# Performance work log

Measured on AMD Instinct MI355X. Metric: run time of the kernel, lower is better.

The kernel has to match this reference:

```python
import jax, jax.numpy as jnp
import numpy as np

NUM_LAYERS = 6
KS = 5  # kernel_size; also attention window size K
EPS_IN = 1e-5  # torch InstanceNorm1d default eps


def _conv1d(x, w, b, d, p):
    # x: [N,C,L], w: [O,I,KS], dilated 'same' conv
    y = jax.lax.conv_general_dilated(x, w, window_strides=(1,), padding=[(p, p)],
                                     rhs_dilation=(d,), dimension_numbers=('NCH', 'OIH', 'NCH'))
    return y + b[None, :, None]


def _pw(x, w, b):
    # pointwise (1x1) conv: x [N,C,L], w [O,C]
    return jnp.einsum('oc,ncl->nol', w, x) + b[None, :, None]


def _layer(x, x_cross, pr, d):
    C, L = x.shape[1], x.shape[2]
    p = (KS // 2) * d  # padding
    conv_w, conv_b, qw, qb, kw, kb, vw, vb, f1w, f1b, f2w, f2b = pr
    out1 = _conv1d(x, conv_w, conv_b, d, p)
    xc = jnp.concatenate([x, x_cross], axis=1)
    q = _pw(xc, qw, qb)            # [N,C,L]
    k = _pw(xc, kw, kb)
    v = _pw(x, vw, vb)
    kp = jnp.pad(k, ((0, 0), (0, 0), (p, p)))
    vp = jnp.pad(v, ((0, 0), (0, 0), (p, p)))
    # attn index for query q, slot j is (q + j*d) into padded axis -> shifted slices
    win_k = jnp.stack([kp[:, :, j * d:j * d + L] for j in range(KS)], axis=-1)  # [N,C,L,K]
    win_v = jnp.stack([vp[:, :, j * d:j * d + L] for j in range(KS)], axis=-1)
    att = jnp.einsum('ncl,nclk->nlk', q, win_k) / np.float32(np.sqrt(C))
    pos = jnp.arange(L)[:, None] + (jnp.arange(KS)[None, :] - KS // 2) * d  # absolute key pos
    mask = (pos >= 0) & (pos < L)  # [L,K]
    att = jax.nn.softmax(att + jnp.log(mask + 1e-6), axis=-1) * mask
    r = jnp.einsum('nlk,nclk->ncl', att, win_v)
    h = out1 + r
    # InstanceNorm1d (no affine): normalize over L per (n,c)
    mu = jnp.mean(h, axis=2, keepdims=True)
    var = jnp.var(h, axis=2, keepdims=True)
    h = (h - mu) * jax.lax.rsqrt(var + EPS_IN)
    out = _pw(jax.nn.relu(_pw(h, f1w, f1b)), f2w, f2b)
    return x + out


def reference(x, x_cross, time_emb, time_w, time_b, conv_w, conv_b, qw, qb, kw, kb, vw, vb, f1w, f1b, f2w, f2b):
    te = time_emb * jax.nn.sigmoid(time_emb)  # swish
    x = x + (te @ time_w.T + time_b)[:, :, None]
    for i in range(NUM_LAYERS):
        pr = (conv_w[i], conv_b[i], qw[i], qb[i], kw[i], kb[i], vw[i], vb[i],
              f1w[i], f1b[i], f2w[i], f2b[i])
        x = _layer(x, x_cross, pr, 2 ** i)
    return x


def setup_inputs() -> dict:
    N, C, CC, L, T, nL = 4, 256, 256, 4096, 512, NUM_LAYERS
    key = jax.random.key(0)
    ks = jax.random.split(key, 18)
    s = 0.05
    return {
        'x': jax.random.normal(ks[0], (N, C, L), jnp.float32),
        'x_cross': jax.random.normal(ks[1], (N, CC, L), jnp.float32),
        'time_emb': jax.random.normal(ks[2], (N, T), jnp.float32),
        'time_w': jax.random.normal(ks[3], (C, T), jnp.float32) * s,
        'time_b': jax.random.normal(ks[4], (C,), jnp.float32) * s,
        'conv_w': jax.random.normal(ks[5], (nL, C, C, KS), jnp.float32) * s,
        'conv_b': jax.random.normal(ks[6], (nL, C), jnp.float32) * s,
        'qw': jax.random.normal(ks[7], (nL, C, C + CC), jnp.float32) * s,
        'qb': jax.random.normal(ks[8], (nL, C), jnp.float32) * s,
        'kw': jax.random.normal(ks[9], (nL, C, C + CC), jnp.float32) * s,
        'kb': jax.random.normal(ks[10], (nL, C), jnp.float32) * s,
        'vw': jax.random.normal(ks[11], (nL, C, C), jnp.float32) * s,
        'vb': jax.random.normal(ks[12], (nL, C), jnp.float32) * s,
        'f1w': jax.random.normal(ks[13], (nL, C, C), jnp.float32) * s,
        'f1b': jax.random.normal(ks[14], (nL, C), jnp.float32) * s,
        'f2w': jax.random.normal(ks[15], (nL, C, C), jnp.float32) * s,
        'f2b': jax.random.normal(ks[16], (nL, C), jnp.float32) * s,
    }
```

## Files before the change

kernel.cpp:

```cpp
#include <hip/hip_runtime.h>
#include <hip/hip_bf16.h>
#include <cstddef>
#include <cstdint>

#define N_   4
#define C_   256
#define L_   4096
#define T_   512
#define KS_  5
#define NL_  6
#define HALO 64
#define LP_  (L_ + 2 * HALO)
#define XCS  512
#define NCH  256

typedef __attribute__((ext_vector_type(8))) __bf16 bf16x8;
typedef __attribute__((ext_vector_type(4))) float f32x4;

#define VM_WAIT4 asm volatile("s_waitcnt vmcnt(4)" ::: "memory")
#define VM_WAIT0 asm volatile("s_waitcnt vmcnt(0)" ::: "memory")

__device__ __forceinline__ void gload_lds16(const void* g, void* l) {
    __builtin_amdgcn_global_load_lds(
        (const __attribute__((address_space(1))) unsigned int*)g,
        (__attribute__((address_space(3))) unsigned int*)l, 16, 0, 0);
}
__device__ __forceinline__ float bf2f(unsigned short u) {
    union { unsigned int i; float f; } x; x.i = ((unsigned int)u) << 16; return x.f;
}
__device__ __forceinline__ unsigned short f2bf(float f) {
    __hip_bfloat16 h = __float2bfloat16(f);
    return *reinterpret_cast<unsigned short*>(&h);
}
__device__ __forceinline__ float4 ld4bf(const unsigned short* p) {
    ushort4 u = *reinterpret_cast<const ushort4*>(p);
    return make_float4(bf2f(u.x), bf2f(u.y), bf2f(u.z), bf2f(u.w));
}

__device__ __forceinline__ void load_frags(
    const unsigned short* As, const unsigned short* Bs,
    int wr, int wc, int lane, bf16x8 af[4], bf16x8 bfr[4])
{
    const int rsel = lane & 15, ksel = (lane >> 4) * 8;
    #pragma unroll
    for (int m = 0; m < 4; m++)
        af[m] = *reinterpret_cast<const bf16x8*>(&As[(wr * 64 + m * 16 + rsel) * 32 + ksel]);
    #pragma unroll
    for (int nn = 0; nn < 4; nn++)
        bfr[nn] = *reinterpret_cast<const bf16x8*>(&Bs[(wc * 64 + nn * 16 + rsel) * 32 + ksel]);
}
__device__ __forceinline__ void mfma16(bf16x8 af[4], bf16x8 bfr[4], f32x4 acc[4][4])
{
    #pragma unroll
    for (int m = 0; m < 4; m++)
        #pragma unroll
        for (int nn = 0; nn < 4; nn++)
            acc[m][nn] = __builtin_amdgcn_mfma_f32_16x16x32_bf16(af[m], bfr[nn], acc[m][nn], 0, 0, 0);
}

__global__ __launch_bounds__(256) void gemm_cq(
    const unsigned short* __restrict__ xcat,
    const unsigned short* __restrict__ wqkv, const float* __restrict__ qkvbias,
    const unsigned short* __restrict__ wconv, const float* __restrict__ cbias,
    unsigned short* __restrict__ qkvb, unsigned short* __restrict__ convb, int d)
{
    __shared__ alignas(16) unsigned short As[3][128 * 32];
    __shared__ alignas(16) unsigned short Bs[3][128 * 32];
    const int tid = threadIdx.x, wid = tid >> 6, lane = tid & 63;
    const int wr = wid >> 1, wc = wid & 1;
    const int r0 = blockIdx.x * 128;
    const int n = r0 >> 12, lb = r0 & (L_ - 1);
    const int s0 = wid * 64 + lane;
    const int ob = blockIdx.y;
    const bool isconv = (ob < 2);
    f32x4 acc[4][4] = {};
    const int orow = (lane >> 4) * 4, ocol = lane & 15;

    if (isconv) {
        const int o0 = ob * 128;
        auto stage = [&](int t, int b) {
            const int tap = t >> 3, kb = (t & 7) * 32;
            const size_t abase = (size_t)((long)n * LP_ + HALO + lb + (tap - 2) * d) * XCS;
            const unsigned short* Wj = wconv + (size_t)tap * C_ * C_;
            #pragma unroll
            for (int i = 0; i < 2; i++) {
                const int s = s0 + i * 256, row = s >> 2, seg = s & 3;
                gload_lds16(xcat + abase + (size_t)row * XCS + kb + seg * 8, As[b] + s * 8);
                gload_lds16(Wj + (size_t)(o0 + row) * C_ + kb + seg * 8, Bs[b] + s * 8);
            }
        };
        const int NT = 40;
        stage(0, 0); stage(1, 1);
        VM_WAIT4;
        __builtin_amdgcn_s_barrier();
        for (int t = 0; t < NT; t++) {
            const int cur = t % 3;
            bf16x8 af[4], bfr[4];
            load_frags(As[cur], Bs[cur], wr, wc, lane, af, bfr);
            if (t + 2 < NT) stage(t + 2, (t + 2) % 3);
            mfma16(af, bfr, acc);
            if (t + 2 < NT) { VM_WAIT4; } else { VM_WAIT0; }
            __builtin_amdgcn_s_barrier();
        }
        #pragma unroll
        for (int m = 0; m < 4; m++)
            #pragma unroll
            for (int nn = 0; nn < 4; nn++) {
                const int gr0 = r0 + wr * 64 + m * 16 + orow;
                const int gc = o0 + wc * 64 + nn * 16 + ocol;
                const float bv = cbias[gc];
                #pragma unroll
                for (int rr = 0; rr < 4; rr++)
                    convb[(size_t)(gr0 + rr) * C_ + gc] = f2bf(acc[m][nn][rr] + bv);
            }
    } else {
        const int o0 = (ob - 2) * 128;
        const size_t abase = ((size_t)n * LP_ + HALO + lb) * XCS;
        auto stage = [&](int t, int b) {
            const int kb = t * 32;
            #pragma unroll
            for (int i = 0; i < 2; i++) {
                const int s = s0 + i * 256, row = s >> 2, seg = s & 3;
                gload_lds16(xcat + abase + (size_t)row * XCS + kb + seg * 8, As[b] + s * 8);
                gload_lds16(wqkv + (size_t)(o0 + row) * 512 + kb + seg * 8, Bs[b] + s * 8);
            }
        };
        const int NT = (o0 >= 512) ? 8 : 16;
        stage(0, 0); stage(1, 1);
        VM_WAIT4;
        __builtin_amdgcn_s_barrier();
        for (int t = 0; t < NT; t++) {
            const int cur = t % 3;
            bf16x8 af[4], bfr[4];
            load_frags(As[cur], Bs[cur], wr, wc, lane, af, bfr);
            if (t + 2 < NT) stage(t + 2, (t + 2) % 3);
            mfma16(af, bfr, acc);
            if (t + 2 < NT) { VM_WAIT4; } else { VM_WAIT0; }
            __builtin_amdgcn_s_barrier();
        }
        #pragma unroll
        for (int m = 0; m < 4; m++)
            #pragma unroll
            for (int nn = 0; nn < 4; nn++) {
                const int gr0 = r0 + wr * 64 + m * 16 + orow;
                const int gc = o0 + wc * 64 + nn * 16 + ocol;
                const float bv = qkvbias[gc];
                #pragma unroll
                for (int rr = 0; rr < 4; rr++)
                    qkvb[(size_t)(gr0 + rr) * 768 + gc] = f2bf(acc[m][nn][rr] + bv);
            }
    }
}

template <int EP, int PERN>
__global__ __launch_bounds__(256) void gemm_std(
    const unsigned short* __restrict__ A,
    const unsigned short* __restrict__ B,
    const float* __restrict__ bias,
    unsigned short* __restrict__ outb,
    float* __restrict__ xres, unsigned short* __restrict__ xcat)
{
    __shared__ alignas(16) unsigned short As[3][128 * 32];
    __shared__ alignas(16) unsigned short Bs[3][128 * 32];
    const int tid = threadIdx.x, wid = tid >> 6, lane = tid & 63;
    const int wr = wid >> 1, wc = wid & 1;
    const int r0 = blockIdx.x * 128;
    const int o0 = blockIdx.y * 128;
    const int n = r0 >> 12;
    if (PERN) {
        B += (size_t)n * C_ * C_;
        bias += n * C_;
    }
    const size_t abase = (size_t)r0 * C_;
    const int s0 = wid * 64 + lane;
    f32x4 acc[4][4] = {};
    auto stage = [&](int t, int b) {
        const int kb = t * 32;
        #pragma unroll
        for (int i = 0; i < 2; i++) {
            const int s = s0 + i * 256, row = s >> 2, seg = s & 3;
            gload_lds16(A + abase + (size_t)row * C_ + kb + seg * 8, As[b] + s * 8);
            gload_lds16(B + (size_t)(o0 + row) * C_ + kb + seg * 8, Bs[b] + s * 8);
        }
    };
    const int NT = 8;
    stage(0, 0); stage(1, 1);
    VM_WAIT4;
    __builtin_amdgcn_s_barrier();
    for (int t = 0; t < NT; t++) {
        const int cur = t % 3;
        bf16x8 af[4], bfr[4];
        load_frags(As[cur], Bs[cur], wr, wc, lane, af, bfr);
        if (t + 2 < NT) stage(t + 2, (t + 2) % 3);
        mfma16(af, bfr, acc);
        if (t + 2 < NT) { VM_WAIT4; } else { VM_WAIT0; }
        __builtin_amdgcn_s_barrier();
    }
    const int orow = (lane >> 4) * 4, ocol = lane & 15;
    #pragma unroll
    for (int m = 0; m < 4; m++)
        #pragma unroll
        for (int nn = 0; nn < 4; nn++) {
            const int gr0 = r0 + wr * 64 + m * 16 + orow;
            const int gc = o0 + wc * 64 + nn * 16 + ocol;
            const float bv = bias[gc];
            #pragma unroll
            for (int rr = 0; rr < 4; rr++) {
                const int gr = gr0 + rr;
                const float v = acc[m][nn][rr] + bv;
                if (EP == 2) {
                    outb[(size_t)gr * C_ + gc] = f2bf(fmaxf(v, 0.f));
                } else {
                    const float nv = v + xres[(size_t)gr * C_ + gc];
                    xres[(size_t)gr * C_ + gc] = nv;
                    const int n2 = gr >> 12, ll = gr & (L_ - 1);
                    xcat[((size_t)n2 * LP_ + HALO + ll) * XCS + gc] = f2bf(nv);
                }
            }
        }
}

__global__ __launch_bounds__(256) void attn_fused(
    const unsigned short* __restrict__ qkv, const unsigned short* __restrict__ convb,
    unsigned short* __restrict__ hb2, float* __restrict__ psum, float* __restrict__ psq, int d)
{
    __shared__ float ps[4][256], pq[4][256];
    const int n = blockIdx.y;
    const int wave = threadIdx.x >> 6;
    const int lane = threadIdx.x & 63;
    float acs[4] = {0.f, 0.f, 0.f, 0.f}, acq[4] = {0.f, 0.f, 0.f, 0.f};
    for (int lq = 0; lq < 4; lq++) {
        const int l = blockIdx.x * 16 + wave * 4 + lq;
        const float4 qv = ld4bf(qkv + ((size_t)n * L_ + l) * 768 + lane * 4);
        float att[KS_];
        #pragma unroll
        for (int j = 0; j < KS_; j++) {
            const int lp = l + (j - 2) * d;
            float s = 0.f;
            if (lp >= 0 && lp < L_) {
                const float4 kv = ld4bf(qkv + ((size_t)n * L_ + lp) * 768 + 256 + lane * 4);
                s = qv.x * kv.x + qv.y * kv.y + qv.z * kv.z + qv.w * kv.w;
            }
            #pragma unroll
            for (int off = 32; off > 0; off >>= 1) s += __shfl_xor(s, off, 64);
            att[j] = s * 0.0625f;
        }
        float logit[KS_], m = -1e30f;
        #pragma unroll
        for (int j = 0; j < KS_; j++) {
            const int lp = l + (j - 2) * d;
            logit[j] = att[j] + logf(((lp >= 0 && lp < L_) ? 1.f : 0.f) + 1e-6f);
            m = fmaxf(m, logit[j]);
        }
        float den = 0.f, wgt[KS_];
        #pragma unroll
        for (int j = 0; j < KS_; j++) { wgt[j] = expf(logit[j] - m); den += wgt[j]; }
        const float inv = 1.f / den;
        float4 r = {0.f, 0.f, 0.f, 0.f};
        #pragma unroll
        for (int j = 0; j < KS_; j++) {
            const int lp = l + (j - 2) * d;
            if (lp < 0 || lp >= L_) continue;
            const float wj = wgt[j] * inv;
            const float4 vv = ld4bf(qkv + ((size_t)n * L_ + lp) * 768 + 512 + lane * 4);
            r.x += wj * vv.x; r.y += wj * vv.y; r.z += wj * vv.z; r.w += wj * vv.w;
        }
        const size_t rowoff = ((size_t)n * L_ + l) * C_ + lane * 4;
        const float4 cv = ld4bf(convb + rowoff);
        const float h0 = cv.x + r.x, h1 = cv.y + r.y, h2 = cv.z + r.z, h3 = cv.w + r.w;
        ushort4 ho;
        ho.x = f2bf(h0); ho.y = f2bf(h1); ho.z = f2bf(h2); ho.w = f2bf(h3);
        *(ushort4*)(hb2 + rowoff) = ho;
        acs[0] += h0; acs[1] += h1; acs[2] += h2; acs[3] += h3;
        acq[0] += h0 * h0; acq[1] += h1 * h1; acq[2] += h2 * h2; acq[3] += h3 * h3;
    }
    const int cb4 = lane * 4;
    #pragma unroll
    for (int u = 0; u < 4; u++) { ps[wave][cb4 + u] = acs[u]; pq[wave][cb4 + u] = acq[u]; }
    __syncthreads();
    const int t = threadIdx.x;
    psum[((size_t)n * NCH + blockIdx.x) * C_ + t] = ps[0][t] + ps[1][t] + ps[2][t] + ps[3][t];
    psq[((size_t)n * NCH + blockIdx.x) * C_ + t] = pq[0][t] + pq[1][t] + pq[2][t] + pq[3][t];
}

__global__ __launch_bounds__(256) void norm_red(
    const float* __restrict__ psum, const float* __restrict__ psq,
    float* __restrict__ psum2, float* __restrict__ psq2)
{
    const int g = blockIdx.x, n = blockIdx.y, c = threadIdx.x;
    float s = 0.f, ss = 0.f;
    for (int ch = g * 16; ch < g * 16 + 16; ch++) {
        s += psum[((size_t)n * NCH + ch) * C_ + c];
        ss += psq[((size_t)n * NCH + ch) * C_ + c];
    }
    psum2[((size_t)n * 16 + g) * C_ + c] = s;
    psq2[((size_t)n * 16 + g) * C_ + c] = ss;
}

__global__ __launch_bounds__(256) void fold_f1(
    const float* __restrict__ f1w, const float* __restrict__ f1b,
    const float* __restrict__ psum2, const float* __restrict__ psq2,
    unsigned short* __restrict__ W1p, float* __restrict__ b1eff)
{
    const int b = blockIdx.x;
    const int n = b >> 8, o = b & 255;
    const int c = threadIdx.x;
    const int lane = c & 63, wid = c >> 6;
    float s = 0.f, ss = 0.f;
    #pragma unroll
    for (int g = 0; g < 16; g++) {
        s += psum2[((size_t)n * 16 + g) * C_ + c];
        ss += psq2[((size_t)n * 16 + g) * C_ + c];
    }
    const float mu = s * (1.f / L_);
    const float scv = rsqrtf(ss * (1.f / L_) - mu * mu + 1e-5f);
    const float w = f1w[o * C_ + c];
    W1p[((size_t)n * C_ + o) * C_ + c] = f2bf(w * scv);
    float part = w * mu * scv;
    #pragma unroll
    for (int off = 32; off > 0; off >>= 1) part += __shfl_xor(part, off, 64);
    __shared__ float red[4];
    if (lane == 0) red[wid] = part;
    __syncthreads();
    if (c == 0) b1eff[n * C_ + o] = f1b[o] - (red[0] + red[1] + red[2] + red[3]);
}

__global__ __launch_bounds__(128) void time_bias_kernel(
    const float* __restrict__ te, const float* __restrict__ tw,
    const float* __restrict__ tb, float* __restrict__ bias)
{
    int nc = blockIdx.x;
    int n = nc >> 8, c = nc & 255;
    int tid = threadIdx.x;
    float s = 0.f;
    for (int t = tid; t < T_; t += 128) {
        float e = te[n * T_ + t];
        s += (e / (1.f + expf(-e))) * tw[c * T_ + t];
    }
    __shared__ float red[128];
    red[tid] = s;
    __syncthreads();
    for (int off = 64; off > 0; off >>= 1) {
        if (tid < off) red[tid] += red[tid + off];
        __syncthreads();
    }
    if (tid == 0) bias[nc] = red[0] + tb[c];
}

__global__ __launch_bounds__(256) void halo_zero(unsigned short* __restrict__ xcat)
{
    const int t = blockIdx.x * 256 + threadIdx.x;
    const int n = t >> 14, rr = (t >> 7) & 127, c4 = t & 127;
    const int row = (rr < 64) ? rr : (L_ + HALO) + (rr - 64);
    ushort4 z = {0, 0, 0, 0};
    *(ushort4*)(xcat + ((size_t)n * LP_ + row) * XCS + c4 * 4) = z;
}

template <int MODE>
__global__ __launch_bounds__(256) void transpose_in(
    const float* __restrict__ in, const float* __restrict__ bias,
    float* __restrict__ xres, unsigned short* __restrict__ xcat)
{
    __shared__ float tile[32][33];
    const int n = blockIdx.z;
    const int l0 = blockIdx.x * 32, c0 = blockIdx.y * 32;
    const int tx = threadIdx.x, ty = threadIdx.y;
    #pragma unroll
    for (int i = 0; i < 4; i++) {
        int c = c0 + ty + 8 * i;
        tile[ty + 8 * i][tx] = in[((size_t)n * C_ + c) * L_ + l0 + tx];
    }
    __syncthreads();
    #pragma unroll
    for (int i = 0; i < 4; i++) {
        const int l = l0 + ty + 8 * i;
        const int c = c0 + tx;
        float v = tile[tx][ty + 8 * i];
        if (MODE == 0) {
            v += bias[n * C_ + c];
            xres[((size_t)n * L_ + l) * C_ + c] = v;
            xcat[((size_t)n * LP_ + HALO + l) * XCS + c] = f2bf(v);
        } else {
            xcat[((size_t)n * LP_ + HALO + l) * XCS + C_ + c] = f2bf(v);
        }
    }
}

__global__ __launch_bounds__(256) void transpose_out(
    const float* __restrict__ in, float* __restrict__ out)
{
    __shared__ float tile[32][33];
    const int n = blockIdx.z;
    const int l0 = blockIdx.x * 32, c0 = blockIdx.y * 32;
    const int tx = threadIdx.x, ty = threadIdx.y;
    #pragma unroll
    for (int i = 0; i < 4; i++) {
        int l = l0 + ty + 8 * i;
        tile[ty + 8 * i][tx] = in[((size_t)n * L_ + l) * C_ + c0 + tx];
    }
    __syncthreads();
    #pragma unroll
    for (int i = 0; i < 4; i++) {
        int c = c0 + ty + 8 * i;
        out[((size_t)n * C_ + c) * L_ + l0 + tx] = tile[tx][ty + 8 * i];
    }
}

__global__ __launch_bounds__(256) void prep_qkv(
    const float* __restrict__ qw, const float* __restrict__ kw, const float* __restrict__ vw,
    const float* __restrict__ qb, const float* __restrict__ kb, const float* __restrict__ vb,
    unsigned short* __restrict__ W, float* __restrict__ Bias)
{
    const size_t idx = (size_t)blockIdx.x * 256 + threadIdx.x;
    const int layer = (int)(idx / (768 * 512));
    const int rem = (int)(idx % (768 * 512));
    const int row = rem >> 9, k = rem & 511;
    float v;
    if (row < 256) v = qw[((size_t)layer * 256 + row) * 512 + k];
    else if (row < 512) v = kw[((size_t)layer * 256 + row - 256) * 512 + k];
    else v = (k < 256) ? vw[((size_t)layer * 256 + row - 512) * 256 + k] : 0.f;
    W[idx] = f2bf(v);
    if (k == 0) {
        float b;
        if (row < 256) b = qb[layer * 256 + row];
        else if (row < 512) b = kb[layer * 256 + row - 256];
        else b = vb[layer * 256 + row - 512];
        Bias[layer * 768 + row] = b;
    }
}

__global__ __launch_bounds__(256) void prep_conv(
    const float* __restrict__ cw, unsigned short* __restrict__ W)
{
    const size_t idx = (size_t)blockIdx.x * 256 + threadIdx.x;
    const int layer = (int)(idx / (KS_ * C_ * C_));
    const int rem = (int)(idx % (KS_ * C_ * C_));
    const int j = rem / (C_ * C_);
    const int o = (rem / C_) & 255, c = rem & 255;
    W[idx] = f2bf(cw[(((size_t)layer * C_ + o) * C_ + c) * KS_ + j]);
}

__global__ __launch_bounds__(256) void conv_f2bf(
    const float* __restrict__ in, unsigned short* __restrict__ out, int nelem)
{
    const int idx = blockIdx.x * 256 + threadIdx.x;
    if (idx < nelem) out[idx] = f2bf(in[idx]);
}

extern "C" void kernel_launch(void* const* d_in, const int* in_sizes, int n_in,
                              void* d_out, int out_size, void* d_ws, size_t ws_size,
                              hipStream_t stream)
{
    (void)in_sizes; (void)n_in; (void)out_size; (void)ws_size;
    const float* x   = (const float*)d_in[0];
    const float* xc  = (const float*)d_in[1];
    const float* te  = (const float*)d_in[2];
    const float* tw  = (const float*)d_in[3];
    const float* tb  = (const float*)d_in[4];
    const float* cw  = (const float*)d_in[5];
    const float* cb  = (const float*)d_in[6];
    const float* qw  = (const float*)d_in[7];
    const float* qbi = (const float*)d_in[8];
    const float* kw  = (const float*)d_in[9];
    const float* kbi = (const float*)d_in[10];
    const float* vw  = (const float*)d_in[11];
    const float* vbi = (const float*)d_in[12];
    const float* f1w = (const float*)d_in[13];
    const float* f1b = (const float*)d_in[14];
    const float* f2w = (const float*)d_in[15];
    const float* f2b = (const float*)d_in[16];

    char* p = (char*)d_ws;
    auto alloc = [&](size_t bytes) { char* r = p; p += (bytes + 255) & ~(size_t)255; return r; };
    const size_t NLC = (size_t)N_ * L_ * C_;
    float* xres  = (float*)alloc(NLC * 4);
    unsigned short* xcat  = (unsigned short*)alloc((size_t)N_ * LP_ * XCS * 2);
    unsigned short* qkvb  = (unsigned short*)alloc((size_t)N_ * L_ * 768 * 2);
    unsigned short* convb = (unsigned short*)alloc(NLC * 2);
    unsigned short* hb2   = (unsigned short*)alloc(NLC * 2);
    unsigned short* f1ob  = (unsigned short*)alloc(NLC * 2);
    unsigned short* wqkvb = (unsigned short*)alloc((size_t)NL_ * 768 * 512 * 2);
    unsigned short* wconvb= (unsigned short*)alloc((size_t)NL_ * KS_ * C_ * C_ * 2);
    unsigned short* wf2b  = (unsigned short*)alloc((size_t)NL_ * C_ * C_ * 2);
    unsigned short* W1p   = (unsigned short*)alloc((size_t)N_ * C_ * C_ * 2);
    float* b1eff  = (float*)alloc((size_t)N_ * C_ * 4);
    float* qkvbias = (float*)alloc((size_t)NL_ * 768 * 4);
    float* biasb = (float*)alloc(N_ * C_ * 4);
    float* psum  = (float*)alloc((size_t)N_ * NCH * C_ * 4);
    float* psq   = (float*)alloc((size_t)N_ * NCH * C_ * 4);
    float* psum2 = (float*)alloc((size_t)N_ * 16 * C_ * 4);
    float* psq2  = (float*)alloc((size_t)N_ * 16 * C_ * 4);

    halo_zero<<<256, 256, 0, stream>>>(xcat);
    prep_qkv<<<(NL_ * 768 * 512) / 256, 256, 0, stream>>>(qw, kw, vw, qbi, kbi, vbi, wqkvb, qkvbias);
    prep_conv<<<(NL_ * KS_ * C_ * C_) / 256, 256, 0, stream>>>(cw, wconvb);
    conv_f2bf<<<(NL_ * C_ * C_) / 256, 256, 0, stream>>>(f2w, wf2b, NL_ * C_ * C_);

    time_bias_kernel<<<N_ * C_, 128, 0, stream>>>(te, tw, tb, biasb);
    dim3 tgrid(L_ / 32, C_ / 32, N_), tblk(32, 8);
    transpose_in<0><<<tgrid, tblk, 0, stream>>>(x, biasb, xres, xcat);
    transpose_in<1><<<tgrid, tblk, 0, stream>>>(xc, nullptr, nullptr, xcat);

    for (int i = 0; i < NL_; i++) {
        const int d = 1 << i;
        gemm_cq<<<dim3(128, 8), 256, 0, stream>>>(
            xcat, wqkvb + (size_t)i * 768 * 512, qkvbias + i * 768,
            wconvb + (size_t)i * KS_ * C_ * C_, cb + i * C_, qkvb, convb, d);
        attn_fused<<<dim3(L_ / 16, N_), 256, 0, stream>>>(qkvb, convb, hb2, psum, psq, d);
        norm_red<<<dim3(16, N_), 256, 0, stream>>>(psum, psq, psum2, psq2);
        fold_f1<<<N_ * C_, 256, 0, stream>>>(
            f1w + (size_t)i * C_ * C_, f1b + i * C_, psum2, psq2, W1p, b1eff);
        gemm_std<2, 1><<<dim3(128, 2), 256, 0, stream>>>(
            hb2, W1p, b1eff, f1ob, nullptr, nullptr);
        gemm_std<3, 0><<<dim3(128, 2), 256, 0, stream>>>(
            f1ob, wf2b + (size_t)i * C_ * C_, f2b + i * C_, nullptr, xres, xcat);
    }
    transpose_out<<<tgrid, tblk, 0, stream>>>(xres, (float*)d_out);
}
```

Measured before the change: 510.7 us.

## Fuse FFN GEMMs into one kernel and swizzle LDS tiles

Merges the two pointwise FFN GEMMs into a single kernel. Each block computes a 64-row tile of relu(h·W1+b1) across all 256 channels, keeps it in LDS as bf16, then multiplies by W2 and applies the residual epilogue. This removes the f1ob round trip through global memory and one launch per layer. It also adds an XOR swizzle to the LDS staging layout in all GEMMs to reduce bank conflicts on fragment loads. In exchange, the FFN grid shrinks to 256 blocks with a larger LDS footprint, which may lower occupancy and limit parallelism.

```diff
diff --git a/kernel.cpp b/kernel.cpp
--- a/kernel.cpp
+++ b/kernel.cpp
@@ -17,6 +17,7 @@
 typedef __attribute__((ext_vector_type(8))) __bf16 bf16x8;
 typedef __attribute__((ext_vector_type(4))) float f32x4;
 
+#define VM_WAIT5 asm volatile("s_waitcnt vmcnt(5)" ::: "memory")
 #define VM_WAIT4 asm volatile("s_waitcnt vmcnt(4)" ::: "memory")
 #define VM_WAIT0 asm volatile("s_waitcnt vmcnt(0)" ::: "memory")
 
@@ -36,18 +37,23 @@
     ushort4 u = *reinterpret_cast<const ushort4*>(p);
     return make_float4(bf2f(u.x), bf2f(u.y), bf2f(u.z), bf2f(u.w));
 }
+__device__ __forceinline__ int swz(int row, int seg) { return seg ^ ((row >> 1) & 3); }
 
 __device__ __forceinline__ void load_frags(
     const unsigned short* As, const unsigned short* Bs,
     int wr, int wc, int lane, bf16x8 af[4], bf16x8 bfr[4])
 {
-    const int rsel = lane & 15, ksel = (lane >> 4) * 8;
-    #pragma unroll
-    for (int m = 0; m < 4; m++)
-        af[m] = *reinterpret_cast<const bf16x8*>(&As[(wr * 64 + m * 16 + rsel) * 32 + ksel]);
-    #pragma unroll
-    for (int nn = 0; nn < 4; nn++)
-        bfr[nn] = *reinterpret_cast<const bf16x8*>(&Bs[(wc * 64 + nn * 16 + rsel) * 32 + ksel]);
+    const int rsel = lane & 15, j = lane >> 4;
+    #pragma unroll
+    for (int m = 0; m < 4; m++) {
+        const int r = wr * 64 + m * 16 + rsel;
+        af[m] = *reinterpret_cast<const bf16x8*>(&As[r * 32 + swz(r, j) * 8]);
+    }
+    #pragma unroll
+    for (int nn = 0; nn < 4; nn++) {
+        const int r = wc * 64 + nn * 16 + rsel;
+        bfr[nn] = *reinterpret_cast<const bf16x8*>(&Bs[r * 32 + swz(r, j) * 8]);
+    }
 }
 __device__ __forceinline__ void mfma16(bf16x8 af[4], bf16x8 bfr[4], f32x4 acc[4][4])
 {
@@ -85,8 +91,9 @@
             #pragma unroll
             for (int i = 0; i < 2; i++) {
                 const int s = s0 + i * 256, row = s >> 2, seg = s & 3;
-                gload_lds16(xcat + abase + (size_t)row * XCS + kb + seg * 8, As[b] + s * 8);
-                gload_lds16(Wj + (size_t)(o0 + row) * C_ + kb + seg * 8, Bs[b] + s * 8);
+                const int gso = swz(row, seg) * 8;
+                gload_lds16(xcat + abase + (size_t)row * XCS + kb + gso, As[b] + s * 8);
+                gload_lds16(Wj + (size_t)(o0 + row) * C_ + kb + gso, Bs[b] + s * 8);
             }
         };
         const int NT = 40;
@@ -121,8 +128,9 @@
             #pragma unroll
             for (int i = 0; i < 2; i++) {
                 const int s = s0 + i * 256, row = s >> 2, seg = s & 3;
-                gload_lds16(xcat + abase + (size_t)row * XCS + kb + seg * 8, As[b] + s * 8);
-                gload_lds16(wqkv + (size_t)(o0 + row) * 512 + kb + seg * 8, Bs[b] + s * 8);
+                const int gso = swz(row, seg) * 8;
+                gload_lds16(xcat + abase + (size_t)row * XCS + kb + gso, As[b] + s * 8);
+                gload_lds16(wqkv + (size_t)(o0 + row) * 512 + kb + gso, Bs[b] + s * 8);
             }
         };
         const int NT = (o0 >= 512) ? 8 : 16;
@@ -152,70 +160,120 @@
     }
 }
 
-template <int EP, int PERN>
-__global__ __launch_bounds__(256) void gemm_std(
-    const unsigned short* __restrict__ A,
-    const unsigned short* __restrict__ B,
-    const float* __restrict__ bias,
-    unsigned short* __restrict__ outb,
+__global__ __launch_bounds__(256) void gemm_ffn(
+    const unsigned short* __restrict__ hb2, const unsigned short* __restrict__ W1p,
+    const float* __restrict__ b1eff, const unsigned short* __restrict__ wf2,
+    const float* __restrict__ f2bias,
     float* __restrict__ xres, unsigned short* __restrict__ xcat)
 {
-    __shared__ alignas(16) unsigned short As[3][128 * 32];
-    __shared__ alignas(16) unsigned short Bs[3][128 * 32];
+    __shared__ alignas(16) unsigned short lds[40960];
     const int tid = threadIdx.x, wid = tid >> 6, lane = tid & 63;
-    const int wr = wid >> 1, wc = wid & 1;
-    const int r0 = blockIdx.x * 128;
-    const int o0 = blockIdx.y * 128;
+    const int r0 = blockIdx.x * 64;
     const int n = r0 >> 12;
-    if (PERN) {
-        B += (size_t)n * C_ * C_;
-        bias += n * C_;
-    }
-    const size_t abase = (size_t)r0 * C_;
-    const int s0 = wid * 64 + lane;
+    const unsigned short* W1 = W1p + (size_t)n * C_ * C_;
+    const int orow = (lane >> 4) * 4, ocol = lane & 15;
+    const int rsel = lane & 15, j = lane >> 4;
+
+    auto stage1 = [&](int t, int b) {
+        const int kb = t * 32;
+        {
+            const int row = tid >> 2, seg = tid & 3;
+            gload_lds16(hb2 + (size_t)(r0 + row) * C_ + kb + swz(row, seg) * 8,
+                        lds + b * 10240 + tid * 8);
+        }
+        #pragma unroll
+        for (int i = 0; i < 4; i++) {
+            const int s = tid + i * 256, row = s >> 2, seg = s & 3;
+            gload_lds16(W1 + (size_t)row * C_ + kb + swz(row, seg) * 8,
+                        lds + b * 10240 + 2048 + s * 8);
+        }
+    };
     f32x4 acc[4][4] = {};
-    auto stage = [&](int t, int b) {
+    stage1(0, 0); stage1(1, 1);
+    VM_WAIT5;
+    __builtin_amdgcn_s_barrier();
+    for (int t = 0; t < 8; t++) {
+        const unsigned short* A = lds + (t % 3) * 10240;
+        const unsigned short* B = A + 2048;
+        bf16x8 af[4], bfr[4];
+        #pragma unroll
+        for (int m = 0; m < 4; m++) {
+            const int r = m * 16 + rsel;
+            af[m] = *reinterpret_cast<const bf16x8*>(&A[r * 32 + swz(r, j) * 8]);
+        }
+        #pragma unroll
+        for (int nn = 0; nn < 4; nn++) {
+            const int r = wid * 64 + nn * 16 + rsel;
+            bfr[nn] = *reinterpret_cast<const bf16x8*>(&B[r * 32 + swz(r, j) * 8]);
+        }
+        if (t + 2 < 8) stage1(t + 2, (t + 2) % 3);
+        mfma16(af, bfr, acc);
+        if (t + 2 < 8) { VM_WAIT5; } else { VM_WAIT0; }
+        __builtin_amdgcn_s_barrier();
+    }
+    auto stage2 = [&](int t, int b) {
         const int kb = t * 32;
         #pragma unroll
-        for (int i = 0; i < 2; i++) {
-            const int s = s0 + i * 256, row = s >> 2, seg = s & 3;
-            gload_lds16(A + abase + (size_t)row * C_ + kb + seg * 8, As[b] + s * 8);
-            gload_lds16(B + (size_t)(o0 + row) * C_ + kb + seg * 8, Bs[b] + s * 8);
+        for (int i = 0; i < 4; i++) {
+            const int s = tid + i * 256, row = s >> 2, seg = s & 3;
+            gload_lds16(wf2 + (size_t)row * C_ + kb + swz(row, seg) * 8,
+                        lds + 16384 + b * 8192 + s * 8);
         }
     };
-    const int NT = 8;
-    stage(0, 0); stage(1, 1);
-    VM_WAIT4;
+    stage2(0, 0); stage2(1, 1);
+    {
+        const float* b1 = b1eff + n * C_;
+        #pragma unroll
+        for (int m = 0; m < 4; m++)
+            #pragma unroll
+            for (int nn = 0; nn < 4; nn++) {
+                const int col = wid * 64 + nn * 16 + ocol;
+                const float bv = b1[col];
+                const int s32 = col >> 3;
+                #pragma unroll
+                for (int rr = 0; rr < 4; rr++) {
+                    const int row = m * 16 + orow + rr;
+                    const float v = fmaxf(acc[m][nn][rr] + bv, 0.f);
+                    lds[row * 256 + ((s32 ^ ((row >> 1) & 3)) * 8) + (col & 7)] = f2bf(v);
+                }
+            }
+    }
+    asm volatile("s_waitcnt lgkmcnt(0) vmcnt(4)" ::: "memory");
     __builtin_amdgcn_s_barrier();
-    for (int t = 0; t < NT; t++) {
-        const int cur = t % 3;
+    f32x4 acc2[4][4] = {};
+    for (int t = 0; t < 8; t++) {
+        const unsigned short* B = lds + 16384 + (t % 3) * 8192;
+        const int kb = t * 32;
         bf16x8 af[4], bfr[4];
-        load_frags(As[cur], Bs[cur], wr, wc, lane, af, bfr);
-        if (t + 2 < NT) stage(t + 2, (t + 2) % 3);
-        mfma16(af, bfr, acc);
-        if (t + 2 < NT) { VM_WAIT4; } else { VM_WAIT0; }
+        #pragma unroll
+        for (int m = 0; m < 4; m++) {
+            const int r = m * 16 + rsel;
+            const int s32 = (kb >> 3) + j;
+            af[m] = *reinterpret_cast<const bf16x8*>(&lds[r * 256 + ((s32 ^ ((r >> 1) & 3)) * 8)]);
+        }
+        #pragma unroll
+        for (int nn = 0; nn < 4; nn++) {
+            const int r = wid * 64 + nn * 16 + rsel;
+            bfr[nn] = *reinterpret_cast<const bf16x8*>(&B[r * 32 + swz(r, j) * 8]);
+        }
+        if (t + 2 < 8) stage2(t + 2, (t + 2) % 3);
+        mfma16(af, bfr, acc2);
+        if (t + 2 < 8) { VM_WAIT4; } else { VM_WAIT0; }
         __builtin_amdgcn_s_barrier();
     }
-    const int orow = (lane >> 4) * 4, ocol = lane & 15;
     #pragma unroll
     for (int m = 0; m < 4; m++)
         #pragma unroll
         for (int nn = 0; nn < 4; nn++) {
-            const int gr0 = r0 + wr * 64 + m * 16 + orow;
-            const int gc = o0 + wc * 64 + nn * 16 + ocol;
-            const float bv = bias[gc];
+            const int gc = wid * 64 + nn * 16 + ocol;
+            const float bv = f2bias[gc];
             #pragma unroll
             for (int rr = 0; rr < 4; rr++) {
-                const int gr = gr0 + rr;
-                const float v = acc[m][nn][rr] + bv;
-                if (EP == 2) {
-                    outb[(size_t)gr * C_ + gc] = f2bf(fmaxf(v, 0.f));
-                } else {
-                    const float nv = v + xres[(size_t)gr * C_ + gc];
-                    xres[(size_t)gr * C_ + gc] = nv;
-                    const int n2 = gr >> 12, ll = gr & (L_ - 1);
-                    xcat[((size_t)n2 * LP_ + HALO + ll) * XCS + gc] = f2bf(nv);
-                }
+                const int gr = r0 + m * 16 + orow + rr;
+                const float nv = acc2[m][nn][rr] + bv + xres[(size_t)gr * C_ + gc];
+                xres[(size_t)gr * C_ + gc] = nv;
+                const int n2 = gr >> 12, ll = gr & (L_ - 1);
+                xcat[((size_t)n2 * LP_ + HALO + ll) * XCS + gc] = f2bf(nv);
             }
         }
 }
@@ -478,7 +536,6 @@
     unsigned short* qkvb  = (unsigned short*)alloc((size_t)N_ * L_ * 768 * 2);
     unsigned short* convb = (unsigned short*)alloc(NLC * 2);
     unsigned short* hb2   = (unsigned short*)alloc(NLC * 2);
-    unsigned short* f1ob  = (unsigned short*)alloc(NLC * 2);
     unsigned short* wqkvb = (unsigned short*)alloc((size_t)NL_ * 768 * 512 * 2);
     unsigned short* wconvb= (unsigned short*)alloc((size_t)NL_ * KS_ * C_ * C_ * 2);
     unsigned short* wf2b  = (unsigned short*)alloc((size_t)NL_ * C_ * C_ * 2);
@@ -510,10 +567,8 @@
         norm_red<<<dim3(16, N_), 256, 0, stream>>>(psum, psq, psum2, psq2);
         fold_f1<<<N_ * C_, 256, 0, stream>>>(
             f1w + (size_t)i * C_ * C_, f1b + i * C_, psum2, psq2, W1p, b1eff);
-        gemm_std<2, 1><<<dim3(128, 2), 256, 0, stream>>>(
-            hb2, W1p, b1eff, f1ob, nullptr, nullptr);
-        gemm_std<3, 0><<<dim3(128, 2), 256, 0, stream>>>(
-            f1ob, wf2b + (size_t)i * C_ * C_, f2b + i * C_, nullptr, xres, xcat);
+        gemm_ffn<<<256, 256, 0, stream>>>(
+            hb2, W1p, b1eff, wf2b + (size_t)i * C_ * C_, f2b + i * C_, xres, xcat);
     }
     transpose_out<<<tgrid, tblk, 0, stream>>>(xres, (float*)d_out);
 }
```

After: 485.0 us. -5.0%, faster.

## Swizzle LDS tiles and retile conv/QKV and FFN GEMMs

Applied to the files above, without the earlier changes.

Adds an XOR swizzle on the 16-byte segment index for LDS tile writes and fragment reads, to cut LDS bank conflicts in the MFMA fragment loads. The conv/QKV GEMM moves to 512-thread blocks with a 256-row A tile, so each weight tile is reused across more rows. The FFN GEMMs shrink to 64-row tiles, doubling block count for better CU occupancy. Wait counts are adjusted to the new number of loads per stage. The trade-offs are more LDS per block and fewer resident blocks for the conv kernel.

```diff
diff --git a/kernel.cpp b/kernel.cpp
--- a/kernel.cpp
+++ b/kernel.cpp
@@ -17,7 +17,7 @@
 typedef __attribute__((ext_vector_type(8))) __bf16 bf16x8;
 typedef __attribute__((ext_vector_type(4))) float f32x4;
 
-#define VM_WAIT4 asm volatile("s_waitcnt vmcnt(4)" ::: "memory")
+#define VM_WAIT3 asm volatile("s_waitcnt vmcnt(3)" ::: "memory")
 #define VM_WAIT0 asm volatile("s_waitcnt vmcnt(0)" ::: "memory")
 
 __device__ __forceinline__ void gload_lds16(const void* g, void* l) {
@@ -36,19 +36,8 @@
     ushort4 u = *reinterpret_cast<const ushort4*>(p);
     return make_float4(bf2f(u.x), bf2f(u.y), bf2f(u.z), bf2f(u.w));
 }
-
-__device__ __forceinline__ void load_frags(
-    const unsigned short* As, const unsigned short* Bs,
-    int wr, int wc, int lane, bf16x8 af[4], bf16x8 bfr[4])
-{
-    const int rsel = lane & 15, ksel = (lane >> 4) * 8;
-    #pragma unroll
-    for (int m = 0; m < 4; m++)
-        af[m] = *reinterpret_cast<const bf16x8*>(&As[(wr * 64 + m * 16 + rsel) * 32 + ksel]);
-    #pragma unroll
-    for (int nn = 0; nn < 4; nn++)
-        bfr[nn] = *reinterpret_cast<const bf16x8*>(&Bs[(wc * 64 + nn * 16 + rsel) * 32 + ksel]);
-}
+__device__ __forceinline__ int swz(int row, int seg) { return seg ^ ((row >> 1) & 3); }
+
 __device__ __forceinline__ void mfma16(bf16x8 af[4], bf16x8 bfr[4], f32x4 acc[4][4])
 {
     #pragma unroll
@@ -58,23 +47,37 @@
             acc[m][nn] = __builtin_amdgcn_mfma_f32_16x16x32_bf16(af[m], bfr[nn], acc[m][nn], 0, 0, 0);
 }
 
-__global__ __launch_bounds__(256) void gemm_cq(
+__global__ __launch_bounds__(512) void gemm_cq(
     const unsigned short* __restrict__ xcat,
     const unsigned short* __restrict__ wqkv, const float* __restrict__ qkvbias,
     const unsigned short* __restrict__ wconv, const float* __restrict__ cbias,
     unsigned short* __restrict__ qkvb, unsigned short* __restrict__ convb, int d)
 {
-    __shared__ alignas(16) unsigned short As[3][128 * 32];
+    __shared__ alignas(16) unsigned short As[3][256 * 32];
     __shared__ alignas(16) unsigned short Bs[3][128 * 32];
     const int tid = threadIdx.x, wid = tid >> 6, lane = tid & 63;
     const int wr = wid >> 1, wc = wid & 1;
-    const int r0 = blockIdx.x * 128;
+    const int r0 = blockIdx.x * 256;
     const int n = r0 >> 12, lb = r0 & (L_ - 1);
-    const int s0 = wid * 64 + lane;
     const int ob = blockIdx.y;
     const bool isconv = (ob < 2);
     f32x4 acc[4][4] = {};
     const int orow = (lane >> 4) * 4, ocol = lane & 15;
+    const int rsel = lane & 15, j = lane >> 4;
+
+    auto read_frags = [&](const unsigned short* A, const unsigned short* B,
+                          bf16x8 af[4], bf16x8 bfr[4]) {
+        #pragma unroll
+        for (int m = 0; m < 4; m++) {
+            const int r = wr * 64 + m * 16 + rsel;
+            af[m] = *reinterpret_cast<const bf16x8*>(&A[r * 32 + swz(r, j) * 8]);
+        }
+        #pragma unroll
+        for (int nn = 0; nn < 4; nn++) {
+            const int r = wc * 64 + nn * 16 + rsel;
+            bfr[nn] = *reinterpret_cast<const bf16x8*>(&B[r * 32 + swz(r, j) * 8]);
+        }
+    };
 
     if (isconv) {
         const int o0 = ob * 128;
@@ -84,22 +87,27 @@
             const unsigned short* Wj = wconv + (size_t)tap * C_ * C_;
             #pragma unroll
             for (int i = 0; i < 2; i++) {
-                const int s = s0 + i * 256, row = s >> 2, seg = s & 3;
-                gload_lds16(xcat + abase + (size_t)row * XCS + kb + seg * 8, As[b] + s * 8);
-                gload_lds16(Wj + (size_t)(o0 + row) * C_ + kb + seg * 8, Bs[b] + s * 8);
+                const int s = tid + i * 512, row = s >> 2, seg = s & 3;
+                gload_lds16(xcat + abase + (size_t)row * XCS + kb + swz(row, seg) * 8,
+                            As[b] + s * 8);
+            }
+            {
+                const int row = tid >> 2, seg = tid & 3;
+                gload_lds16(Wj + (size_t)(o0 + row) * C_ + kb + swz(row, seg) * 8,
+                            Bs[b] + tid * 8);
             }
         };
         const int NT = 40;
         stage(0, 0); stage(1, 1);
-        VM_WAIT4;
+        VM_WAIT3;
         __builtin_amdgcn_s_barrier();
         for (int t = 0; t < NT; t++) {
             const int cur = t % 3;
             bf16x8 af[4], bfr[4];
-            load_frags(As[cur], Bs[cur], wr, wc, lane, af, bfr);
+            read_frags(As[cur], Bs[cur], af, bfr);
             if (t + 2 < NT) stage(t + 2, (t + 2) % 3);
             mfma16(af, bfr, acc);
-            if (t + 2 < NT) { VM_WAIT4; } else { VM_WAIT0; }
+            if (t + 2 < NT) { VM_WAIT3; } else { VM_WAIT0; }
             __builtin_amdgcn_s_barrier();
         }
         #pragma unroll
@@ -120,22 +128,27 @@
             const int kb = t * 32;
             #pragma unroll
             for (int i = 0; i < 2; i++) {
-                const int s = s0 + i * 256, row = s >> 2, seg = s & 3;
-                gload_lds16(xcat + abase + (size_t)row * XCS + kb + seg * 8, As[b] + s * 8);
-                gload_lds16(wqkv + (size_t)(o0 + row) * 512 + kb + seg * 8, Bs[b] + s * 8);
+                const int s = tid + i * 512, row = s >> 2, seg = s & 3;
+                gload_lds16(xcat + abase + (size_t)row * XCS + kb + swz(row, seg) * 8,
+                            As[b] + s * 8);
+            }
+            {
+                const int row = tid >> 2, seg = tid & 3;
+                gload_lds16(wqkv + (size_t)(o0 + row) * 512 + kb + swz(row, seg) * 8,
+                            Bs[b] + tid * 8);
             }
         };
         const int NT = (o0 >= 512) ? 8 : 16;
         stage(0, 0); stage(1, 1);
-        VM_WAIT4;
+        VM_WAIT3;
         __builtin_amdgcn_s_barrier();
         for (int t = 0; t < NT; t++) {
             const int cur = t % 3;
             bf16x8 af[4], bfr[4];
-            load_frags(As[cur], Bs[cur], wr, wc, lane, af, bfr);
+            read_frags(As[cur], Bs[cur], af, bfr);
             if (t + 2 < NT) stage(t + 2, (t + 2) % 3);
             mfma16(af, bfr, acc);
-            if (t + 2 < NT) { VM_WAIT4; } else { VM_WAIT0; }
+            if (t + 2 < NT) { VM_WAIT3; } else { VM_WAIT0; }
             __builtin_amdgcn_s_barrier();
         }
         #pragma unroll
@@ -153,18 +166,18 @@
 }
 
 template <int EP, int PERN>
-__global__ __launch_bounds__(256) void gemm_std(
+__global__ __launch_bounds__(256) void gemm_f(
     const unsigned short* __restrict__ A,
     const unsigned short* __restrict__ B,
     const float* __restrict__ bias,
     unsigned short* __restrict__ outb,
     float* __restrict__ xres, unsigned short* __restrict__ xcat)
 {
-    __shared__ alignas(16) unsigned short As[3][128 * 32];
+    __shared__ alignas(16) unsigned short As[3][64 * 32];
     __shared__ alignas(16) unsigned short Bs[3][128 * 32];
     const int tid = threadIdx.x, wid = tid >> 6, lane = tid & 63;
     const int wr = wid >> 1, wc = wid & 1;
-    const int r0 = blockIdx.x * 128;
+    const int r0 = blockIdx.x * 64;
     const int o0 = blockIdx.y * 128;
     const int n = r0 >> 12;
     if (PERN) {
@@ -172,36 +185,52 @@
         bias += n * C_;
     }
     const size_t abase = (size_t)r0 * C_;
-    const int s0 = wid * 64 + lane;
-    f32x4 acc[4][4] = {};
+    const int rsel = lane & 15, j = lane >> 4;
+    f32x4 acc[2][4] = {};
     auto stage = [&](int t, int b) {
         const int kb = t * 32;
+        {
+            const int row = tid >> 2, seg = tid & 3;
+            gload_lds16(A + abase + (size_t)row * C_ + kb + swz(row, seg) * 8, As[b] + tid * 8);
+        }
         #pragma unroll
         for (int i = 0; i < 2; i++) {
-            const int s = s0 + i * 256, row = s >> 2, seg = s & 3;
-            gload_lds16(A + abase + (size_t)row * C_ + kb + seg * 8, As[b] + s * 8);
-            gload_lds16(B + (size_t)(o0 + row) * C_ + kb + seg * 8, Bs[b] + s * 8);
+            const int s = tid + i * 256, row = s >> 2, seg = s & 3;
+            gload_lds16(B + (size_t)(o0 + row) * C_ + kb + swz(row, seg) * 8, Bs[b] + s * 8);
         }
     };
     const int NT = 8;
     stage(0, 0); stage(1, 1);
-    VM_WAIT4;
+    VM_WAIT3;
     __builtin_amdgcn_s_barrier();
     for (int t = 0; t < NT; t++) {
         const int cur = t % 3;
-        bf16x8 af[4], bfr[4];
-        load_frags(As[cur], Bs[cur], wr, wc, lane, af, bfr);
+        bf16x8 af[2], bfr[4];
+        #pragma unroll
+        for (int m = 0; m < 2; m++) {
+            const int r = wr * 32 + m * 16 + rsel;
+            af[m] = *reinterpret_cast<const bf16x8*>(&As[cur][r * 32 + swz(r, j) * 8]);
+        }
+        #pragma unroll
+        for (int nn = 0; nn < 4; nn++) {
+            const int r = wc * 64 + nn * 16 + rsel;
+            bfr[nn] = *reinterpret_cast<const bf16x8*>(&Bs[cur][r * 32 + swz(r, j) * 8]);
+        }
         if (t + 2 < NT) stage(t + 2, (t + 2) % 3);
-        mfma16(af, bfr, acc);
-        if (t + 2 < NT) { VM_WAIT4; } else { VM_WAIT0; }
+        #pragma unroll
+        for (int m = 0; m < 2; m++)
+            #pragma unroll
+            for (int nn = 0; nn < 4; nn++)
+                acc[m][nn] = __builtin_amdgcn_mfma_f32_16x16x32_bf16(af[m], bfr[nn], acc[m][nn], 0, 0, 0);
+        if (t + 2 < NT) { VM_WAIT3; } else { VM_WAIT0; }
         __builtin_amdgcn_s_barrier();
     }
     const int orow = (lane >> 4) * 4, ocol = lane & 15;
     #pragma unroll
-    for (int m = 0; m < 4; m++)
+    for (int m = 0; m < 2; m++)
         #pragma unroll
         for (int nn = 0; nn < 4; nn++) {
-            const int gr0 = r0 + wr * 64 + m * 16 + orow;
+            const int gr0 = r0 + wr * 32 + m * 16 + orow;
             const int gc = o0 + wc * 64 + nn * 16 + ocol;
             const float bv = bias[gc];
             #pragma unroll
@@ -503,16 +532,16 @@
 
     for (int i = 0; i < NL_; i++) {
         const int d = 1 << i;
-        gemm_cq<<<dim3(128, 8), 256, 0, stream>>>(
+        gemm_cq<<<dim3(64, 8), 512, 0, stream>>>(
             xcat, wqkvb + (size_t)i * 768 * 512, qkvbias + i * 768,
             wconvb + (size_t)i * KS_ * C_ * C_, cb + i * C_, qkvb, convb, d);
         attn_fused<<<dim3(L_ / 16, N_), 256, 0, stream>>>(qkvb, convb, hb2, psum, psq, d);
         norm_red<<<dim3(16, N_), 256, 0, stream>>>(psum, psq, psum2, psq2);
         fold_f1<<<N_ * C_, 256, 0, stream>>>(
             f1w + (size_t)i * C_ * C_, f1b + i * C_, psum2, psq2, W1p, b1eff);
-        gemm_std<2, 1><<<dim3(128, 2), 256, 0, stream>>>(
+        gemm_f<2, 1><<<dim3(256, 2), 256, 0, stream>>>(
             hb2, W1p, b1eff, f1ob, nullptr, nullptr);
-        gemm_std<3, 0><<<dim3(128, 2), 256, 0, stream>>>(
+        gemm_f<3, 0><<<dim3(256, 2), 256, 0, stream>>>(
             f1ob, wf2b + (size_t)i * C_ * C_, f2b + i * C_, nullptr, xres, xcat);
     }
     transpose_out<<<tgrid, tblk, 0, stream>>>(xres, (float*)d_out);
```

New measurement: 496.8 us. 1.03x faster.
